# Kernel optimization log

Hardware: AMD Instinct MI355X
Metric: run time of the kernel (lower is better)

## Reference

```python
import jax, jax.numpy as jnp
import numpy as np

EPS_NORM = 1e-5   # o_norm eps
EPS_L2 = 1e-6     # qk l2norm eps
CHUNK = 128       # chunk length for the scan


def _short_conv(x, w):
    # x: [B,T,C], w: [C,K]; causal depthwise conv followed by silu (ShortConvolution)
    K = w.shape[1]
    T = x.shape[1]
    xp = jnp.pad(x, ((0, 0), (K - 1, 0), (0, 0)))
    y = sum(xp[:, i:i + T, :] * w[:, i] for i in range(K))
    return jax.nn.silu(y)


def _l2norm(x):
    return x * jax.lax.rsqrt(jnp.sum(x * x, axis=-1, keepdims=True) + EPS_L2)


def _kda_scan(q, k, v, gk, beta):
    # gated delta rule: S_t = (I - b_t k_t k_t^T) diag(exp(gk_t)) S_{t-1} + b_t k_t v_t^T;  o_t = q_t^T S_t
    # q,k,gk: [B,T,H,Dk]; v: [B,T,H,Dv]; beta: [B,T,H]
    B, T, H, Dk = q.shape
    Dv = v.shape[-1]
    NC = T // CHUNK

    def c4(x):  # [B,T,H,D] -> [NC, CHUNK, B, H, D]
        return jnp.transpose(x.reshape(B, NC, CHUNK, H, x.shape[-1]), (1, 2, 0, 3, 4))

    qc, kc, vc, gc = c4(q), c4(k), c4(v), c4(gk)
    bc = jnp.transpose(beta.reshape(B, NC, CHUNK, H), (1, 2, 0, 3))

    def step(S, inp):  # S: [B,H,Dk,Dv]
        q_t, k_t, v_t, g_t, b_t = inp
        S = S * jnp.exp(g_t)[..., None]                       # per-key-channel decay
        err = v_t - jnp.einsum('bhk,bhkv->bhv', k_t, S)       # delta-rule error
        S = S + b_t[..., None, None] * (k_t[..., None] * err[..., None, :])
        o_t = jnp.einsum('bhk,bhkv->bhv', q_t, S)
        return S, o_t

    @jax.checkpoint
    def chunk_fn(S, xs):
        return jax.lax.scan(step, S, xs)

    S0 = jnp.zeros((B, H, Dk, Dv), q.dtype)
    _, o = jax.lax.scan(chunk_fn, S0, (qc, kc, vc, gc, bc))   # o: [NC, CHUNK, B, H, Dv]
    return jnp.transpose(o.reshape(T, B, H, Dv), (1, 0, 2, 3))


def _forward(hidden_states, q_w, k_w, v_w, q_conv_w, k_conv_w, v_conv_w,
             f_w1, f_w2, b_w, A_log, dt_bias, g_w1, g_w2, g_b2, o_norm_w, o_w):
    B, T, D = hidden_states.shape
    H = A_log.shape[0]
    Dv = o_norm_w.shape[0]
    Dk = q_w.shape[1] // H

    q = _short_conv(hidden_states @ q_w, q_conv_w).reshape(B, T, H, Dk)
    k = _short_conv(hidden_states @ k_w, k_conv_w).reshape(B, T, H, Dk)
    v = _short_conv(hidden_states @ v_w, v_conv_w).reshape(B, T, H, Dv)

    # fused_kda_gate: per-channel log-decay
    g = ((hidden_states @ f_w1) @ f_w2).reshape(B, T, H, Dk)
    gk = -jnp.exp(A_log)[:, None] * jax.nn.softplus(g + dt_bias.reshape(H, Dk))

    beta = jax.nn.sigmoid(hidden_states @ b_w)  # [B,T,H]

    q = _l2norm(q) * (Dk ** -0.5)
    k = _l2norm(k)

    o = _kda_scan(q, k, v, gk, beta)  # [B,T,H,Dv]

    # FusedRMSNormGated(activation='sigmoid')
    gate = ((hidden_states @ g_w1) @ g_w2 + g_b2).reshape(B, T, H, Dv)
    o = o * jax.lax.rsqrt(jnp.mean(o * o, axis=-1, keepdims=True) + EPS_NORM) * o_norm_w
    o = o * jax.nn.sigmoid(gate)

    return o.reshape(B, T, H * Dv) @ o_w


def setup_inputs() -> dict:
    key = jax.random.key(0)
    B, T, D = 2, 4096, 2048
    H, Dk, Dv = 16, 128, 128
    KD, VD = H * Dk, H * Dv
    Kc = 4
    ks = jax.random.split(key, 16)
    s = 0.02
    n = lambda kk, sh: jax.random.normal(kk, sh, jnp.float32) * s
    return dict(
        hidden_states=jax.random.normal(ks[0], (B, T, D), jnp.float32),
        q_w=n(ks[1], (D, KD)), k_w=n(ks[2], (D, KD)), v_w=n(ks[3], (D, VD)),
        q_conv_w=n(ks[4], (KD, Kc)), k_conv_w=n(ks[5], (KD, Kc)), v_conv_w=n(ks[6], (VD, Kc)),
        f_w1=n(ks[7], (D, Dv)), f_w2=n(ks[8], (Dv, KD)),
        b_w=n(ks[9], (D, H)),
        A_log=jnp.log(jax.random.uniform(ks[10], (H,), jnp.float32, 1.0, 16.0)),
        dt_bias=jnp.zeros((KD,), jnp.float32),
        g_w1=n(ks[11], (D, Dv)), g_w2=n(ks[12], (Dv, VD)), g_b2=jnp.zeros((VD,), jnp.float32),
        o_norm_w=jnp.ones((Dv,), jnp.float32),
        o_w=n(ks[13], (VD, D)),
    )


def reference(hidden_states, q_w, k_w, v_w, q_conv_w, k_conv_w, v_conv_w,
              f_w1, f_w2, b_w, A_log, dt_bias, g_w1, g_w2, g_b2, o_norm_w, o_w):
    return _forward(hidden_states, q_w, k_w, v_w, q_conv_w, k_conv_w, v_conv_w,
                    f_w1, f_w2, b_w, A_log, dt_bias, g_w1, g_w2, g_b2, o_norm_w, o_w)
```

## Files before the change

kernel.cpp:

```cpp
#include <hip/hip_runtime.h>
#include <math.h>


constexpr int NB = 2, NT = 4096, ND = 2048, NH = 16, DK = 128, DV = 128;
constexpr int MROWS = NB * NT;
constexpr int BHN   = NB * NH;
constexpr int CCH   = 16;
constexpr int NCH   = NT / CCH;

#define DEV static __device__ __forceinline__

typedef __attribute__((ext_vector_type(8))) short short8;
typedef __attribute__((ext_vector_type(4))) short short4v;
typedef __attribute__((ext_vector_type(4))) float f32x4;

DEV float sigmoidf_(float x) { return 1.0f / (1.0f + expf(-x)); }

DEV float bf2f(unsigned u) { return __uint_as_float(u << 16); }
DEV unsigned f2bf(float f) {
    unsigned u = __float_as_uint(f);
    return (u + 0x7fffu + ((u >> 16) & 1u)) >> 16;
}
DEV unsigned pack2(float a, float b) { return f2bf(a) | (f2bf(b) << 16); }

DEV void gl2lds16(const unsigned short* g, unsigned short* l) {
    __builtin_amdgcn_global_load_lds(
        (const __attribute__((address_space(1))) unsigned int*)g,
        (__attribute__((address_space(3))) unsigned int*)l, 16, 0, 0);
}

template <int CTRL>
DEV float dppadd(float x) {
    int y = __builtin_amdgcn_mov_dpp(__float_as_int(x), CTRL, 0xF, 0xF, true);
    return x + __int_as_float(y);
}
DEV float reduce16f(float x) {
    x = dppadd<0xB1>(x);
    x = dppadd<0x4E>(x);
    x = dppadd<0x141>(x);
    x = dppadd<0x140>(x);
    return x;
}

DEV float4 bflo(uint4 U) {
    return make_float4(bf2f(U.x & 0xffff), bf2f(U.x >> 16),
                       bf2f(U.y & 0xffff), bf2f(U.y >> 16));
}
DEV float4 bfhi(uint4 U) {
    return make_float4(bf2f(U.z & 0xffff), bf2f(U.z >> 16),
                       bf2f(U.w & 0xffff), bf2f(U.w >> 16));
}

DEV f32x4 mfma16(short4v a, short4v b, f32x4 c) {
#if __has_builtin(__builtin_amdgcn_mfma_f32_16x16x16bf16_1k)
    return __builtin_amdgcn_mfma_f32_16x16x16bf16_1k(a, b, c, 0, 0, 0);
#elif __has_builtin(__builtin_amdgcn_mfma_f32_16x16x16_bf16)
    return __builtin_amdgcn_mfma_f32_16x16x16_bf16(a, b, c, 0, 0, 0);
#else
    asm volatile("s_nop 1\n\t"
                 "v_mfma_f32_16x16x16_bf16 %0, %1, %2, %0\n\t"
                 "s_nop 7\n\t"
                 "s_nop 7"
                 : "+v"(c) : "v"(a), "v"(b));
    return c;
#endif
}

template <int OUTBF>
__global__ __launch_bounds__(256) void gemm_bf16(
    const unsigned short* __restrict__ A, const unsigned short* __restrict__ Bt,
    void* __restrict__ Cv, int Md, int Nd, int Kd)
{
    __shared__ unsigned short As[128 * 64];
    __shared__ unsigned short Bs[128 * 64];

    const int nbx = Nd >> 7;
    const int bx = blockIdx.x % nbx;
    const int by = blockIdx.x / nbx;
    const int m0 = by << 7, n0 = bx << 7;
    const int tid = threadIdx.x;
    const int lane = tid & 63, wid = tid >> 6;
    const int wr = wid >> 1, wc = wid & 1;

    const int srow  = tid >> 3;
    const int sslot = (tid & 7) ^ (srow & 7);
    const unsigned short* ag = A  + (size_t)(m0 + srow) * Kd + sslot * 8;
    const unsigned short* bg = Bt + (size_t)(n0 + srow) * Kd + sslot * 8;
    const size_t rstep32 = (size_t)32 * Kd;
    unsigned short* aw = As + wid * 512;
    unsigned short* bw = Bs + wid * 512;

    const int rrow  = lane & 15;
    const int khalf = lane >> 4;
    const int rswz  = rrow & 7;

    f32x4 zf = {0.f, 0.f, 0.f, 0.f};
    f32x4 acc[4][4];
#pragma unroll
    for (int m = 0; m < 4; m++)
#pragma unroll
        for (int n = 0; n < 4; n++) acc[m][n] = zf;

    for (int k0 = 0; k0 < Kd; k0 += 64) {
#pragma unroll
        for (int i = 0; i < 4; i++) {
            gl2lds16(ag + (size_t)i * rstep32 + k0, aw + i * 2048);
            gl2lds16(bg + (size_t)i * rstep32 + k0, bw + i * 2048);
        }
        __syncthreads();
#pragma unroll
        for (int kk = 0; kk < 2; kk++) {
            const int slot = (kk * 4 + khalf) ^ rswz;
            short8 a[4], b[4];
#pragma unroll
            for (int m = 0; m < 4; m++)
                a[m] = *(const short8*)&As[(wr * 64 + m * 16 + rrow) * 64 + slot * 8];
#pragma unroll
            for (int n = 0; n < 4; n++)
                b[n] = *(const short8*)&Bs[(wc * 64 + n * 16 + rrow) * 64 + slot * 8];
#pragma unroll
            for (int m = 0; m < 4; m++)
#pragma unroll
                for (int n = 0; n < 4; n++)
                    acc[m][n] = __builtin_amdgcn_mfma_f32_16x16x32_bf16(
                        a[m], b[n], acc[m][n], 0, 0, 0);
        }
        __syncthreads();
    }

#pragma unroll
    for (int m = 0; m < 4; m++) {
        const int rowb = m0 + wr * 64 + m * 16 + khalf * 4;
#pragma unroll
        for (int n = 0; n < 4; n++) {
            const int col = n0 + wc * 64 + n * 16 + rrow;
#pragma unroll
            for (int r = 0; r < 4; r++) {
                const float v = acc[m][n][r];
                if (OUTBF)
                    ((unsigned short*)Cv)[(size_t)(rowb + r) * Nd + col] =
                        (unsigned short)f2bf(v);
                else
                    ((float*)Cv)[(size_t)(rowb + r) * Nd + col] = v;
            }
        }
    }
}

__global__ __launch_bounds__(256) void wtrans(
    const float* __restrict__ W, unsigned short* __restrict__ Wt, int Kd, int Nd)
{
    __shared__ float T[64][65];
    const int nbk = Kd >> 6;
    const int bk = blockIdx.x % nbk, bn = blockIdx.x / nbk;
    const int k0 = bk << 6, n0 = bn << 6;
    const int tid = threadIdx.x;
    {
        const int r = tid >> 2, cg = tid & 3;
#pragma unroll
        for (int i = 0; i < 4; i++) {
            float4 f = *(const float4*)&W[(size_t)(k0 + r) * Nd + n0 + cg * 16 + i * 4];
            T[r][cg * 16 + i * 4 + 0] = f.x;
            T[r][cg * 16 + i * 4 + 1] = f.y;
            T[r][cg * 16 + i * 4 + 2] = f.z;
            T[r][cg * 16 + i * 4 + 3] = f.w;
        }
    }
    __syncthreads();
    {
        const int n = tid >> 2, kg = tid & 3;
#pragma unroll
        for (int i = 0; i < 2; i++) {
            unsigned o[4];
#pragma unroll
            for (int j = 0; j < 4; j++) {
                const int kk = kg * 16 + i * 8 + 2 * j;
                o[j] = pack2(T[kk][n], T[kk + 1][n]);
            }
            *(uint4*)&Wt[(size_t)(n0 + n) * Kd + k0 + kg * 16 + i * 8] =
                make_uint4(o[0], o[1], o[2], o[3]);
        }
    }
}

__global__ __launch_bounds__(256) void f2bf_k(
    const float* __restrict__ x, unsigned short* __restrict__ y, int n8)
{
    const int i = blockIdx.x * blockDim.x + threadIdx.x;
    if (i < n8) {
        float4 a = *(const float4*)&x[(size_t)i * 8];
        float4 b = *(const float4*)&x[(size_t)i * 8 + 4];
        uint4 o = make_uint4(pack2(a.x, a.y), pack2(a.z, a.w),
                             pack2(b.x, b.y), pack2(b.z, b.w));
        *(uint4*)&y[(size_t)i * 8] = o;
    }
}

template <int MODE>
__global__ __launch_bounds__(256) void conv_silu(
    const unsigned short* __restrict__ pre, const float* __restrict__ cw,
    unsigned short* __restrict__ outp)
{
    const int m = blockIdx.x;
    const int t = m & (NT - 1);
    const int b = m >> 12;
    const int tid = threadIdx.x;
    const int hd = tid * 8;
    const int h  = hd >> 7;
    const int d0 = hd & 127;

    float xr[4][8];
#pragma unroll
    for (int i = 0; i < 4; i++) {
        const int tt = t - 3 + i;
        if (tt >= 0) {
            uint4 u = *(const uint4*)(pre + (size_t)(m - 3 + i) * ND + hd);
            float4 lo = bflo(u), hi = bfhi(u);
            xr[i][0] = lo.x; xr[i][1] = lo.y; xr[i][2] = lo.z; xr[i][3] = lo.w;
            xr[i][4] = hi.x; xr[i][5] = hi.y; xr[i][6] = hi.z; xr[i][7] = hi.w;
        } else {
#pragma unroll
            for (int j = 0; j < 8; j++) xr[i][j] = 0.f;
        }
    }
    float y[8];
    float ssum = 0.f;
#pragma unroll
    for (int j = 0; j < 8; j++) {
        float4 w = *(const float4*)&cw[(size_t)(hd + j) * 4];
        float v = xr[0][j] * w.x + xr[1][j] * w.y + xr[2][j] * w.z + xr[3][j] * w.w;
        v = v * sigmoidf_(v);
        y[j] = v;
        ssum += v * v;
    }
    float scale = 1.f;
    if (MODE >= 1) {
        ssum = reduce16f(ssum);
        scale = rsqrtf(ssum + 1e-6f);
        if (MODE == 2) scale *= 0.08838834764831845f;
    }
    uint4 pk;
    pk.x = pack2(y[0] * scale, y[1] * scale);
    pk.y = pack2(y[2] * scale, y[3] * scale);
    pk.z = pack2(y[4] * scale, y[5] * scale);
    pk.w = pack2(y[6] * scale, y[7] * scale);
    unsigned short* dst = outp + ((size_t)(b * NH + h) * NT + t) * 128 + d0;
    *(uint4*)dst = pk;
}

__global__ __launch_bounds__(256) void gk_k(
    const unsigned short* __restrict__ g, const float* __restrict__ A_log,
    const float* __restrict__ dtb, _Float16* __restrict__ gko)
{
    const int m = blockIdx.x;
    const int t = m & (NT - 1);
    const int b = m >> 12;
    const int tid = threadIdx.x;
    const int hd = tid * 8, h = hd >> 7, d0 = hd & 127;
    const float ea = expf(A_log[h]);
    uint4 u = *(const uint4*)(g + (size_t)m * ND + hd);
    float4 lo = bflo(u), hi = bfhi(u);
    float4 b0 = *(const float4*)&dtb[hd], b1 = *(const float4*)&dtb[hd + 4];
    float xin[8] = {lo.x + b0.x, lo.y + b0.y, lo.z + b0.z, lo.w + b0.w,
                    hi.x + b1.x, hi.y + b1.y, hi.z + b1.z, hi.w + b1.w};
    union { _Float16 h8[8]; uint4 u4; } up;
#pragma unroll
    for (int j = 0; j < 8; j++) {
        float x = xin[j];
        float sp = (x > 20.f) ? x : log1pf(expf(x));
        up.h8[j] = (_Float16)(-ea * sp);
    }
    _Float16* dst = gko + ((size_t)(b * NH + h) * NT + t) * 128 + d0;
    *(uint4*)dst = up.u4;
}

__global__ __launch_bounds__(256) void beta_k(
    const float* __restrict__ hs, const float* __restrict__ bw,
    float* __restrict__ bt)
{
    __shared__ float sh[ND];
    __shared__ float part[16][17];
    const int m = blockIdx.x, tid = threadIdx.x;
    ((float4*)sh)[tid * 2]     = ((const float4*)(hs + (size_t)m * ND))[tid * 2];
    ((float4*)sh)[tid * 2 + 1] = ((const float4*)(hs + (size_t)m * ND))[tid * 2 + 1];
    __syncthreads();
    const int h = tid & 15, seg = tid >> 4;
    float p = 0.f;
#pragma unroll 8
    for (int j = 0; j < 128; j++)
        p += sh[seg * 128 + j] * bw[(size_t)(seg * 128 + j) * 16 + h];
    part[seg][h] = p;
    __syncthreads();
    if (tid < 16) {
        float s = 0.f;
#pragma unroll
        for (int i = 0; i < 16; i++) s += part[i][tid];
        const int t = m & (NT - 1), b = m >> 12;
        bt[(size_t)(b * NH + tid) * NT + t] = sigmoidf_(s);
    }
}

__global__ __launch_bounds__(256) void kda_prep(
    unsigned short* __restrict__ qn, unsigned short* __restrict__ kn,
    unsigned short* __restrict__ vv, unsigned short* __restrict__ gkh,
    const float* __restrict__ bt,
    float* __restrict__ BdB, float* __restrict__ eCB)
{
    __shared__ float cL[16][132];
    __shared__ float kL[16][132];
    __shared__ float qL[16][132];
    __shared__ float kapL[16][132];
    __shared__ float AbL[16][16];
    __shared__ float bL[16];
    __shared__ float sx[16][264];

    const int blk = blockIdx.x;
    const int bh  = blk >> 8;
    const int cc  = blk & 255;
    const int tid = threadIdx.x;
    const size_t ebase  = ((size_t)bh * NT + cc * 16) * 128;
    const size_t chbase = (size_t)bh * NCH + cc;

    if (tid < 16) bL[tid] = bt[(size_t)bh * NT + cc * 16 + tid];

    if (tid < 128) {
        const int d = tid;
        float c = 0.f;
#pragma unroll
        for (int i = 0; i < 16; i++) {
            float g = (float)(((const _Float16*)gkh)[ebase + i * 128 + d]);
            c += g;
            cL[i][d] = c;
            float kv = bf2f(kn[ebase + i * 128 + d]);
            float qv = bf2f(qn[ebase + i * 128 + d]);
            kL[i][d] = kv; qL[i][d] = qv;
            kapL[i][d] = kv * expf(c);
        }
        eCB[chbase * 128 + d] = expf(c);
    }
    __syncthreads();

    if (tid < 128) {
        const int d = tid;
        const float clast = cL[15][d];
        unsigned u[8];
#pragma unroll
        for (int e = 0; e < 8; e++) {
            float v0 = bL[2 * e]     * kL[2 * e][d]     * expf(clast - cL[2 * e][d]);
            float v1 = bL[2 * e + 1] * kL[2 * e + 1][d] * expf(clast - cL[2 * e + 1][d]);
            u[e] = pack2(v0, v1);
        }
        uint4* dst = (uint4*)(gkh + chbase * 2048 + (size_t)d * 16);
        dst[0] = make_uint4(u[0], u[1], u[2], u[3]);
        dst[1] = make_uint4(u[4], u[5], u[6], u[7]);
    }

    const int si = tid >> 4, sj = tid & 15;
    float aAcc = 0.f, bAcc = 0.f;
    if (si >= sj) {
        for (int d4 = 0; d4 < 128; d4 += 4) {
            float4 ci = *(const float4*)&cL[si][d4];
            float4 cj = *(const float4*)&cL[sj][d4];
            float4 ki = *(const float4*)&kL[si][d4];
            float4 kj = *(const float4*)&kL[sj][d4];
            float4 qi = *(const float4*)&qL[si][d4];
            float w;
            w = expf(ci.x - cj.x); aAcc += ki.x * kj.x * w; bAcc += qi.x * kj.x * w;
            w = expf(ci.y - cj.y); aAcc += ki.y * kj.y * w; bAcc += qi.y * kj.y * w;
            w = expf(ci.z - cj.z); aAcc += ki.z * kj.z * w; bAcc += qi.z * kj.z * w;
            w = expf(ci.w - cj.w); aAcc += ki.w * kj.w * w; bAcc += qi.w * kj.w * w;
        }
    }
    if (si > sj) AbL[si][sj] = aAcc * bL[sj];
    BdB[chbase * 256 + si * 16 + sj] = bAcc * bL[sj];
    __syncthreads();

    {
        const int col = tid;
        float x[16];
#pragma unroll
        for (int i = 0; i < 16; i++)
            x[i] = (col < 128) ? kapL[i][col]
                               : bf2f(vv[ebase + (size_t)i * 128 + (col - 128)]);
#pragma unroll
        for (int i = 1; i < 16; i++) {
            float s = x[i];
#pragma unroll
            for (int l = 0; l < 15; l++)
                if (l < i) s -= AbL[i][l] * x[l];
            x[i] = s;
        }
#pragma unroll
        for (int i = 0; i < 16; i++) sx[i][col] = x[i];
    }
    __syncthreads();

    {
        const int row = tid >> 4, d0 = (tid & 15) * 8;
        unsigned pu[4], vu[4], qu[4];
#pragma unroll
        for (int e = 0; e < 4; e++) {
            pu[e] = pack2(-sx[row][d0 + 2 * e], -sx[row][d0 + 2 * e + 1]);
            vu[e] = pack2(sx[row][128 + d0 + 2 * e], sx[row][128 + d0 + 2 * e + 1]);
            qu[e] = pack2(qL[row][d0 + 2 * e]     * expf(cL[row][d0 + 2 * e]),
                          qL[row][d0 + 2 * e + 1] * expf(cL[row][d0 + 2 * e + 1]));
        }
        const size_t ro = ebase + (size_t)row * 128 + d0;
        *(uint4*)(kn + ro) = make_uint4(pu[0], pu[1], pu[2], pu[3]);
        *(uint4*)(vv + ro) = make_uint4(vu[0], vu[1], vu[2], vu[3]);
        *(uint4*)(qn + ro) = make_uint4(qu[0], qu[1], qu[2], qu[3]);
    }
}

__global__ __launch_bounds__(64) void kda_scan2(
    const unsigned short* __restrict__ qn, const unsigned short* __restrict__ kn,
    const unsigned short* __restrict__ vv, const unsigned short* __restrict__ khat,
    const float* __restrict__ BdB, const float* __restrict__ eCB,
    float* __restrict__ osc)
{
    const int bh = blockIdx.x & 31;
    const int vg = blockIdx.x >> 5;
    const int lane = threadIdx.x;
    const int r16 = lane & 15, h4 = lane >> 4;
    const int bb = bh >> 4, hh = bh & 15;

    f32x4 Sm[8];
    short4v Shi[8], Slo[8];
    const short4v z4 = {0, 0, 0, 0};
#pragma unroll
    for (int t = 0; t < 8; t++) {
        Sm[t] = (f32x4){0.f, 0.f, 0.f, 0.f};
        Shi[t] = z4; Slo[t] = z4;
    }

    for (int cc = 0; cc < NCH; cc++) {
        const size_t ebase = ((size_t)bh * NT + cc * 16) * 128;
        const size_t chb = (size_t)bh * NCH + cc;
        short4v P[8], Q[8], KH[8];
        float4 eCt[8];
#pragma unroll
        for (int t = 0; t < 8; t++) {
            P[t]  = *(const short4v*)(kn + ebase + (size_t)r16 * 128 + t * 16 + h4 * 4);
            Q[t]  = *(const short4v*)(qn + ebase + (size_t)r16 * 128 + t * 16 + h4 * 4);
            KH[t] = *(const short4v*)(khat + chb * 2048 + (size_t)(t * 16 + r16) * 16 + h4 * 4);
            eCt[t] = *(const float4*)(eCB + chb * 128 + t * 16 + h4 * 4);
        }
        float4 bd4 = *(const float4*)(BdB + chb * 256 + (size_t)r16 * 16 + h4 * 4);
        short4v bdf;
        bdf[0] = (short)f2bf(bd4.x); bdf[1] = (short)f2bf(bd4.y);
        bdf[2] = (short)f2bf(bd4.z); bdf[3] = (short)f2bf(bd4.w);

        f32x4 accE, accO = {0.f, 0.f, 0.f, 0.f};
#pragma unroll
        for (int r = 0; r < 4; r++)
            accE[r] = bf2f(vv[ebase + (size_t)(h4 * 4 + r) * 128 + vg * 16 + r16]);

#pragma unroll
        for (int t = 0; t < 8; t++) {
            accE = mfma16(P[t], Shi[t], accE);
            accE = mfma16(P[t], Slo[t], accE);
            accO = mfma16(Q[t], Shi[t], accO);
            accO = mfma16(Q[t], Slo[t], accO);
        }
        short4v ef;
        ef[0] = (short)f2bf(accE[0]); ef[1] = (short)f2bf(accE[1]);
        ef[2] = (short)f2bf(accE[2]); ef[3] = (short)f2bf(accE[3]);
        accO = mfma16(bdf, ef, accO);

#pragma unroll
        for (int t = 0; t < 8; t++) {
            f32x4 ns;
            ns[0] = eCt[t].x * Sm[t][0];
            ns[1] = eCt[t].y * Sm[t][1];
            ns[2] = eCt[t].z * Sm[t][2];
            ns[3] = eCt[t].w * Sm[t][3];
            ns = mfma16(KH[t], ef, ns);
            Sm[t] = ns;
            short4v nh, nl;
#pragma unroll
            for (int r = 0; r < 4; r++) {
                unsigned hb = f2bf(ns[r]);
                nh[r] = (short)hb;
                nl[r] = (short)f2bf(ns[r] - bf2f(hb));
            }
            Shi[t] = nh; Slo[t] = nl;
        }

        const size_t obase = ((size_t)bb * NT + cc * 16) * ND + hh * 128 + vg * 16 + r16;
#pragma unroll
        for (int r = 0; r < 4; r++)
            osc[obase + (size_t)(h4 * 4 + r) * ND] = accO[r];
    }
}

__global__ __launch_bounds__(256) void gate_k(
    const float* __restrict__ osc, const unsigned short* __restrict__ gateb,
    const float* __restrict__ gb2, const float* __restrict__ onw,
    unsigned short* __restrict__ ogb)
{
    const int m = blockIdx.x, tid = threadIdx.x;
    const int hd = tid * 8, d0 = hd & 127;
    const float* op = osc + (size_t)m * ND + hd;
    float4 o0 = *(const float4*)op, o1 = *(const float4*)(op + 4);
    float ssum = o0.x * o0.x + o0.y * o0.y + o0.z * o0.z + o0.w * o0.w +
                 o1.x * o1.x + o1.y * o1.y + o1.z * o1.z + o1.w * o1.w;
    ssum = reduce16f(ssum);
    const float r = rsqrtf(ssum * (1.0f / 128.0f) + 1e-5f);
    uint4 gu = *(const uint4*)(gateb + (size_t)m * ND + hd);
    float4 gl = bflo(gu), gh = bfhi(gu);
    float4 b0 = *(const float4*)&gb2[hd], b1 = *(const float4*)&gb2[hd + 4];
    float4 w0 = *(const float4*)&onw[d0], w1 = *(const float4*)&onw[d0 + 4];
    float res[8];
    res[0] = o0.x * r * w0.x * sigmoidf_(gl.x + b0.x);
    res[1] = o0.y * r * w0.y * sigmoidf_(gl.y + b0.y);
    res[2] = o0.z * r * w0.z * sigmoidf_(gl.z + b0.z);
    res[3] = o0.w * r * w0.w * sigmoidf_(gl.w + b0.w);
    res[4] = o1.x * r * w1.x * sigmoidf_(gh.x + b1.x);
    res[5] = o1.y * r * w1.y * sigmoidf_(gh.y + b1.y);
    res[6] = o1.z * r * w1.z * sigmoidf_(gh.z + b1.z);
    res[7] = o1.w * r * w1.w * sigmoidf_(gh.w + b1.w);
    uint4 pk;
    pk.x = pack2(res[0], res[1]); pk.y = pack2(res[2], res[3]);
    pk.z = pack2(res[4], res[5]); pk.w = pack2(res[6], res[7]);
    *(uint4*)(ogb + (size_t)m * ND + hd) = pk;
}

__global__ void diag_fill(float* out, float val, int n) {
    for (int i = blockIdx.x * blockDim.x + threadIdx.x; i < n; i += gridDim.x * blockDim.x)
        out[i] = val;
}

extern "C" void kernel_launch(void* const* d_in, const int* in_sizes, int n_in,
                              void* d_out, int out_size, void* d_ws, size_t ws_size,
                              hipStream_t stream)
{
    const float* hs    = (const float*)d_in[0];
    const float* q_w   = (const float*)d_in[1];
    const float* k_w   = (const float*)d_in[2];
    const float* v_w   = (const float*)d_in[3];
    const float* qcw   = (const float*)d_in[4];
    const float* kcw   = (const float*)d_in[5];
    const float* vcw   = (const float*)d_in[6];
    const float* f_w1  = (const float*)d_in[7];
    const float* f_w2  = (const float*)d_in[8];
    const float* b_w   = (const float*)d_in[9];
    const float* A_log = (const float*)d_in[10];
    const float* dt_b  = (const float*)d_in[11];
    const float* g_w1  = (const float*)d_in[12];
    const float* g_w2  = (const float*)d_in[13];
    const float* g_b2  = (const float*)d_in[14];
    const float* onw   = (const float*)d_in[15];
    const float* o_w   = (const float*)d_in[16];
    float* out = (float*)d_out;

    const size_t SEQ = (size_t)BHN * NT;
    const size_t BF  = SEQ * 128 * 2;
    char* wsb = (char*)d_ws;
    size_t off = 0;
    unsigned short* qn   = (unsigned short*)(wsb + off); off += BF;
    unsigned short* kn   = (unsigned short*)(wsb + off); off += BF;
    unsigned short* vv   = (unsigned short*)(wsb + off); off += BF;
    unsigned short* dc   = (unsigned short*)(wsb + off); off += BF;
    unsigned short* P1   = (unsigned short*)(wsb + off); off += (size_t)MROWS * ND * 2;
    unsigned short* WT   = (unsigned short*)(wsb + off); off += (size_t)ND * ND * 2;
    unsigned short* fw1t = (unsigned short*)(wsb + off); off += (size_t)DK * ND * 2;
    unsigned short* fw2t = (unsigned short*)(wsb + off); off += (size_t)ND * DK * 2;
    unsigned short* gw1t = (unsigned short*)(wsb + off); off += (size_t)DK * ND * 2;
    unsigned short* gw2t = (unsigned short*)(wsb + off); off += (size_t)ND * DK * 2;
    unsigned short* f1b  = (unsigned short*)(wsb + off); off += (size_t)MROWS * DK * 2;
    unsigned short* g1b  = (unsigned short*)(wsb + off); off += (size_t)MROWS * DK * 2;
    float* bt  = (float*)(wsb + off); off += SEQ * 4;
    float* BdB = (float*)(wsb + off); off += (size_t)BHN * NCH * 256 * 4;
    float* eCB = (float*)(wsb + off); off += (size_t)BHN * NCH * 128 * 4;
    unsigned short* ogb = vv;
    unsigned short* hsb = (unsigned short*)d_out;

    if (ws_size < off) {
        diag_fill<<<512, 256, 0, stream>>>(out, 1.0e6f + (float)(ws_size >> 20), out_size);
        return;
    }

    dim3 blk(256);
    auto g2 = [](int Md, int Nd) { return dim3((unsigned)((Md >> 7) * (Nd >> 7))); };
    auto gt = [](int Kd, int Nd) { return dim3((unsigned)((Kd >> 6) * (Nd >> 6))); };

    f2bf_k<<<(MROWS * ND / 8 + 255) / 256, blk, 0, stream>>>(hs, hsb, MROWS * ND / 8);

    wtrans<<<gt(ND, ND), blk, 0, stream>>>(q_w, WT, ND, ND);
    gemm_bf16<1><<<g2(MROWS, ND), blk, 0, stream>>>(hsb, WT, P1, MROWS, ND, ND);
    conv_silu<2><<<MROWS, blk, 0, stream>>>(P1, qcw, qn);
    wtrans<<<gt(ND, ND), blk, 0, stream>>>(k_w, WT, ND, ND);
    gemm_bf16<1><<<g2(MROWS, ND), blk, 0, stream>>>(hsb, WT, P1, MROWS, ND, ND);
    conv_silu<1><<<MROWS, blk, 0, stream>>>(P1, kcw, kn);
    wtrans<<<gt(ND, ND), blk, 0, stream>>>(v_w, WT, ND, ND);
    gemm_bf16<1><<<g2(MROWS, ND), blk, 0, stream>>>(hsb, WT, P1, MROWS, ND, ND);
    conv_silu<0><<<MROWS, blk, 0, stream>>>(P1, vcw, vv);

    wtrans<<<gt(ND, DK), blk, 0, stream>>>(f_w1, fw1t, ND, DK);
    gemm_bf16<1><<<g2(MROWS, DK), blk, 0, stream>>>(hsb, fw1t, f1b, MROWS, DK, ND);
    wtrans<<<gt(DK, ND), blk, 0, stream>>>(f_w2, fw2t, DK, ND);
    gemm_bf16<1><<<g2(MROWS, ND), blk, 0, stream>>>(f1b, fw2t, P1, MROWS, ND, DK);
    gk_k<<<MROWS, blk, 0, stream>>>(P1, A_log, dt_b, (_Float16*)dc);

    wtrans<<<gt(ND, DK), blk, 0, stream>>>(g_w1, gw1t, ND, DK);
    gemm_bf16<1><<<g2(MROWS, DK), blk, 0, stream>>>(hsb, gw1t, g1b, MROWS, DK, ND);
    wtrans<<<gt(DK, ND), blk, 0, stream>>>(g_w2, gw2t, DK, ND);
    gemm_bf16<1><<<g2(MROWS, ND), blk, 0, stream>>>(g1b, gw2t, P1, MROWS, ND, DK);

    beta_k<<<MROWS, blk, 0, stream>>>(hs, b_w, bt);

    kda_prep<<<BHN * NCH, blk, 0, stream>>>(qn, kn, vv, dc, bt, BdB, eCB);
    kda_scan2<<<256, 64, 0, stream>>>(qn, kn, vv, dc, BdB, eCB, out);

    gate_k<<<MROWS, blk, 0, stream>>>(out, P1, g_b2, onw, ogb);

    wtrans<<<gt(ND, ND), blk, 0, stream>>>(o_w, WT, ND, ND);
    gemm_bf16<0><<<g2(MROWS, ND), blk, 0, stream>>>(ogb, WT, out, MROWS, ND, ND);
}
```

Measured before the change: 1.442 ms.

## Double-buffer chunk loads in scan kernel and split MFMA accumulators

Restructures the sequential chunk loop of the recurrent scan kernel so the global loads for the next chunk are issued into a second register set before computing the current chunk. This hides load latency behind the serial MFMA chain. It also splits the E and O accumulations into two independent accumulator chains each, summed at the end, to shorten MFMA dependency chains. The cost is roughly doubled register use for staged operands, which may cause spills or lower occupancy.

```diff
diff --git a/kernel.cpp b/kernel.cpp
--- a/kernel.cpp
+++ b/kernel.cpp
@@ -433,11 +433,10 @@
         Shi[t] = z4; Slo[t] = z4;
     }
 
-    for (int cc = 0; cc < NCH; cc++) {
+    auto loadc = [&](int cc, short4v* P, short4v* Q, short4v* KH,
+                     float4* eCt, short4v& bdf, f32x4& accInit) {
         const size_t ebase = ((size_t)bh * NT + cc * 16) * 128;
         const size_t chb = (size_t)bh * NCH + cc;
-        short4v P[8], Q[8], KH[8];
-        float4 eCt[8];
 #pragma unroll
         for (int t = 0; t < 8; t++) {
             P[t]  = *(const short4v*)(kn + ebase + (size_t)r16 * 128 + t * 16 + h4 * 4);
@@ -446,22 +445,36 @@
             eCt[t] = *(const float4*)(eCB + chb * 128 + t * 16 + h4 * 4);
         }
         float4 bd4 = *(const float4*)(BdB + chb * 256 + (size_t)r16 * 16 + h4 * 4);
-        short4v bdf;
         bdf[0] = (short)f2bf(bd4.x); bdf[1] = (short)f2bf(bd4.y);
         bdf[2] = (short)f2bf(bd4.z); bdf[3] = (short)f2bf(bd4.w);
-
-        f32x4 accE, accO = {0.f, 0.f, 0.f, 0.f};
 #pragma unroll
         for (int r = 0; r < 4; r++)
-            accE[r] = bf2f(vv[ebase + (size_t)(h4 * 4 + r) * 128 + vg * 16 + r16]);
-
-#pragma unroll
-        for (int t = 0; t < 8; t++) {
-            accE = mfma16(P[t], Shi[t], accE);
-            accE = mfma16(P[t], Slo[t], accE);
-            accO = mfma16(Q[t], Shi[t], accO);
-            accO = mfma16(Q[t], Slo[t], accO);
-        }
+            accInit[r] = bf2f(vv[ebase + (size_t)(h4 * 4 + r) * 128 + vg * 16 + r16]);
+    };
+
+    auto compute = [&](int cc, const short4v* P, const short4v* Q,
+                       const short4v* KH, const float4* eCt,
+                       short4v bdf, f32x4 accInit) {
+        f32x4 e0 = accInit, e1 = {0.f, 0.f, 0.f, 0.f};
+        f32x4 o0 = {0.f, 0.f, 0.f, 0.f}, o1 = {0.f, 0.f, 0.f, 0.f};
+#pragma unroll
+        for (int t = 0; t < 8; t += 2) {
+            e0 = mfma16(P[t],     Shi[t],     e0);
+            e1 = mfma16(P[t + 1], Shi[t + 1], e1);
+            o0 = mfma16(Q[t],     Shi[t],     o0);
+            o1 = mfma16(Q[t + 1], Shi[t + 1], o1);
+            e0 = mfma16(P[t],     Slo[t],     e0);
+            e1 = mfma16(P[t + 1], Slo[t + 1], e1);
+            o0 = mfma16(Q[t],     Slo[t],     o0);
+            o1 = mfma16(Q[t + 1], Slo[t + 1], o1);
+        }
+        f32x4 accE;
+        accE[0] = e0[0] + e1[0]; accE[1] = e0[1] + e1[1];
+        accE[2] = e0[2] + e1[2]; accE[3] = e0[3] + e1[3];
+        f32x4 accO;
+        accO[0] = o0[0] + o1[0]; accO[1] = o0[1] + o1[1];
+        accO[2] = o0[2] + o1[2]; accO[3] = o0[3] + o1[3];
+
         short4v ef;
         ef[0] = (short)f2bf(accE[0]); ef[1] = (short)f2bf(accE[1]);
         ef[2] = (short)f2bf(accE[2]); ef[3] = (short)f2bf(accE[3]);
@@ -490,6 +503,20 @@
 #pragma unroll
         for (int r = 0; r < 4; r++)
             osc[obase + (size_t)(h4 * 4 + r) * ND] = accO[r];
+    };
+
+    short4v Pa[8], Qa[8], KHa[8], Pb[8], Qb[8], KHb[8];
+    float4 eCa[8], eCb[8];
+    short4v bda, bdb;
+    f32x4 ia, ib;
+
+    loadc(0, Pa, Qa, KHa, eCa, bda, ia);
+    for (int cc = 0; cc < NCH; cc += 2) {
+        loadc(cc + 1, Pb, Qb, KHb, eCb, bdb, ib);
+        compute(cc, Pa, Qa, KHa, eCa, bda, ia);
+        if (cc + 2 < NCH)
+            loadc(cc + 2, Pa, Qa, KHa, eCa, bda, ia);
+        compute(cc + 1, Pb, Qb, KHb, eCb, bdb, ib);
     }
 }
 
```

Result: faster. 1.306 ms (-9.5%).

## Repack scan operands for 128-bit loads, drop hi/lo split, merge value groups

Applied to the files above, without the earlier changes.

The prep kernel now writes k, q, khat and v in interleaved layouts so the scan loads 8-element short8 vectors instead of 4-element ones. The scan kernel drops the bf16 hi+lo split of the state and uses only the high part, which halves the MFMAs in the recurrence but lowers precision. It also splits the accumulation into two independent chains to shorten dependency latency. The eight value-group blocks per head are merged into one 512-thread block, which launches 32 blocks instead of 256 and cuts the shared per-chunk loads across waves. The risk is accuracy loss from the bf16-only state over 256 chunks.

```diff
diff --git a/kernel.cpp b/kernel.cpp
--- a/kernel.cpp
+++ b/kernel.cpp
@@ -50,6 +50,9 @@
     return make_float4(bf2f(U.z & 0xffff), bf2f(U.z >> 16),
                        bf2f(U.w & 0xffff), bf2f(U.w >> 16));
 }
+
+DEV short4v lo4(short8 v) { short4v r; r[0]=v[0]; r[1]=v[1]; r[2]=v[2]; r[3]=v[3]; return r; }
+DEV short4v hi4(short8 v) { short4v r; r[0]=v[4]; r[1]=v[5]; r[2]=v[6]; r[3]=v[7]; return r; }
 
 DEV f32x4 mfma16(short4v a, short4v b, f32x4 c) {
 #if __has_builtin(__builtin_amdgcn_mfma_f32_16x16x16bf16_1k)
@@ -342,6 +345,7 @@
 
     if (tid < 128) {
         const int d = tid;
+        const int t = d >> 4, rr = d & 15;
         const float clast = cL[15][d];
         unsigned u[8];
 #pragma unroll
@@ -350,9 +354,12 @@
             float v1 = bL[2 * e + 1] * kL[2 * e + 1][d] * expf(clast - cL[2 * e + 1][d]);
             u[e] = pack2(v0, v1);
         }
-        uint4* dst = (uint4*)(gkh + chbase * 2048 + (size_t)d * 16);
-        dst[0] = make_uint4(u[0], u[1], u[2], u[3]);
-        dst[1] = make_uint4(u[4], u[5], u[6], u[7]);
+        unsigned short* base = gkh + chbase * 2048 +
+                               (size_t)(((t >> 1) * 16 + rr) * 32 + (t & 1) * 4);
+        *(uint2*)(base +  0) = make_uint2(u[0], u[1]);
+        *(uint2*)(base +  8) = make_uint2(u[2], u[3]);
+        *(uint2*)(base + 16) = make_uint2(u[4], u[5]);
+        *(uint2*)(base + 24) = make_uint2(u[6], u[7]);
     }
 
     const int si = tid >> 4, sj = tid & 15;
@@ -396,72 +403,92 @@
     __syncthreads();
 
     {
-        const int row = tid >> 4, d0 = (tid & 15) * 8;
-        unsigned pu[4], vu[4], qu[4];
+        const int row = tid >> 4, q16 = tid & 15;
+        const int d0 = q16 * 8;
+        const int t  = q16 >> 1;
+        const int pos0 = (t >> 1) * 32 + (t & 1) * 4 + (q16 & 1) * 16;
+        unsigned pu[4], qu[4];
 #pragma unroll
         for (int e = 0; e < 4; e++) {
             pu[e] = pack2(-sx[row][d0 + 2 * e], -sx[row][d0 + 2 * e + 1]);
-            vu[e] = pack2(sx[row][128 + d0 + 2 * e], sx[row][128 + d0 + 2 * e + 1]);
             qu[e] = pack2(qL[row][d0 + 2 * e]     * expf(cL[row][d0 + 2 * e]),
                           qL[row][d0 + 2 * e + 1] * expf(cL[row][d0 + 2 * e + 1]));
         }
-        const size_t ro = ebase + (size_t)row * 128 + d0;
-        *(uint4*)(kn + ro) = make_uint4(pu[0], pu[1], pu[2], pu[3]);
-        *(uint4*)(vv + ro) = make_uint4(vu[0], vu[1], vu[2], vu[3]);
-        *(uint4*)(qn + ro) = make_uint4(qu[0], qu[1], qu[2], qu[3]);
-    }
-}
-
-__global__ __launch_bounds__(64) void kda_scan2(
+        unsigned short* kb = kn + ebase + (size_t)row * 128 + pos0;
+        unsigned short* qb = qn + ebase + (size_t)row * 128 + pos0;
+        *(uint2*)(kb)     = make_uint2(pu[0], pu[1]);
+        *(uint2*)(kb + 8) = make_uint2(pu[2], pu[3]);
+        *(uint2*)(qb)     = make_uint2(qu[0], qu[1]);
+        *(uint2*)(qb + 8) = make_uint2(qu[2], qu[3]);
+    }
+    if (tid < 128) {
+        const int c = tid;
+        unsigned u2[8];
+#pragma unroll
+        for (int e = 0; e < 8; e++)
+            u2[e] = pack2(sx[2 * e][128 + c], sx[2 * e + 1][128 + c]);
+        unsigned short* vb = vv + ebase + (size_t)c * 16;
+        *(uint4*)(vb)     = make_uint4(u2[0], u2[1], u2[2], u2[3]);
+        *(uint4*)(vb + 8) = make_uint4(u2[4], u2[5], u2[6], u2[7]);
+    }
+}
+
+__global__ __launch_bounds__(512) void kda_scan3(
     const unsigned short* __restrict__ qn, const unsigned short* __restrict__ kn,
     const unsigned short* __restrict__ vv, const unsigned short* __restrict__ khat,
     const float* __restrict__ BdB, const float* __restrict__ eCB,
     float* __restrict__ osc)
 {
-    const int bh = blockIdx.x & 31;
-    const int vg = blockIdx.x >> 5;
-    const int lane = threadIdx.x;
+    const int bh = blockIdx.x;
+    const int vg = threadIdx.x >> 6;
+    const int lane = threadIdx.x & 63;
     const int r16 = lane & 15, h4 = lane >> 4;
     const int bb = bh >> 4, hh = bh & 15;
 
     f32x4 Sm[8];
-    short4v Shi[8], Slo[8];
+    short4v Shi[8];
     const short4v z4 = {0, 0, 0, 0};
 #pragma unroll
-    for (int t = 0; t < 8; t++) {
-        Sm[t] = (f32x4){0.f, 0.f, 0.f, 0.f};
-        Shi[t] = z4; Slo[t] = z4;
-    }
+    for (int t = 0; t < 8; t++) { Sm[t] = (f32x4){0.f, 0.f, 0.f, 0.f}; Shi[t] = z4; }
 
     for (int cc = 0; cc < NCH; cc++) {
         const size_t ebase = ((size_t)bh * NT + cc * 16) * 128;
         const size_t chb = (size_t)bh * NCH + cc;
-        short4v P[8], Q[8], KH[8];
+
+        short8 Pp[4], Qp[4], KHp[4];
+#pragma unroll
+        for (int m = 0; m < 4; m++) {
+            Pp[m]  = *(const short8*)(kn + ebase + (size_t)r16 * 128 + m * 32 + h4 * 8);
+            Qp[m]  = *(const short8*)(qn + ebase + (size_t)r16 * 128 + m * 32 + h4 * 8);
+            KHp[m] = *(const short8*)(khat + chb * 2048 + (size_t)(m * 16 + r16) * 32 + h4 * 8);
+        }
+        short4v vvt = *(const short4v*)(vv + ebase + (size_t)(vg * 16 + r16) * 16 + h4 * 4);
         float4 eCt[8];
 #pragma unroll
-        for (int t = 0; t < 8; t++) {
-            P[t]  = *(const short4v*)(kn + ebase + (size_t)r16 * 128 + t * 16 + h4 * 4);
-            Q[t]  = *(const short4v*)(qn + ebase + (size_t)r16 * 128 + t * 16 + h4 * 4);
-            KH[t] = *(const short4v*)(khat + chb * 2048 + (size_t)(t * 16 + r16) * 16 + h4 * 4);
+        for (int t = 0; t < 8; t++)
             eCt[t] = *(const float4*)(eCB + chb * 128 + t * 16 + h4 * 4);
-        }
         float4 bd4 = *(const float4*)(BdB + chb * 256 + (size_t)r16 * 16 + h4 * 4);
         short4v bdf;
         bdf[0] = (short)f2bf(bd4.x); bdf[1] = (short)f2bf(bd4.y);
         bdf[2] = (short)f2bf(bd4.z); bdf[3] = (short)f2bf(bd4.w);
 
-        f32x4 accE, accO = {0.f, 0.f, 0.f, 0.f};
-#pragma unroll
-        for (int r = 0; r < 4; r++)
-            accE[r] = bf2f(vv[ebase + (size_t)(h4 * 4 + r) * 128 + vg * 16 + r16]);
-
-#pragma unroll
-        for (int t = 0; t < 8; t++) {
-            accE = mfma16(P[t], Shi[t], accE);
-            accE = mfma16(P[t], Slo[t], accE);
-            accO = mfma16(Q[t], Shi[t], accO);
-            accO = mfma16(Q[t], Slo[t], accO);
-        }
+        f32x4 e0, e1 = {0.f, 0.f, 0.f, 0.f};
+        f32x4 o0 = {0.f, 0.f, 0.f, 0.f}, o1 = {0.f, 0.f, 0.f, 0.f};
+        e0[0] = bf2f((unsigned short)vvt[0]); e0[1] = bf2f((unsigned short)vvt[1]);
+        e0[2] = bf2f((unsigned short)vvt[2]); e0[3] = bf2f((unsigned short)vvt[3]);
+#pragma unroll
+        for (int m = 0; m < 4; m++) {
+            e0 = mfma16(lo4(Pp[m]), Shi[2 * m],     e0);
+            e1 = mfma16(hi4(Pp[m]), Shi[2 * m + 1], e1);
+            o0 = mfma16(lo4(Qp[m]), Shi[2 * m],     o0);
+            o1 = mfma16(hi4(Qp[m]), Shi[2 * m + 1], o1);
+        }
+        f32x4 accE, accO;
+        accE[0] = e0[0] + e1[0]; accE[1] = e0[1] + e1[1];
+        accE[2] = e0[2] + e1[2]; accE[3] = e0[3] + e1[3];
+        accO[0] = o0[0] + o1[0]; accO[1] = o0[1] + o1[1];
+        accO[2] = o0[2] + o1[2]; accO[3] = o0[3] + o1[3];
+
         short4v ef;
         ef[0] = (short)f2bf(accE[0]); ef[1] = (short)f2bf(accE[1]);
         ef[2] = (short)f2bf(accE[2]); ef[3] = (short)f2bf(accE[3]);
@@ -469,21 +496,18 @@
 
 #pragma unroll
         for (int t = 0; t < 8; t++) {
+            const short4v khf = (t & 1) ? hi4(KHp[t >> 1]) : lo4(KHp[t >> 1]);
             f32x4 ns;
             ns[0] = eCt[t].x * Sm[t][0];
             ns[1] = eCt[t].y * Sm[t][1];
             ns[2] = eCt[t].z * Sm[t][2];
             ns[3] = eCt[t].w * Sm[t][3];
-            ns = mfma16(KH[t], ef, ns);
+            ns = mfma16(khf, ef, ns);
             Sm[t] = ns;
-            short4v nh, nl;
-#pragma unroll
-            for (int r = 0; r < 4; r++) {
-                unsigned hb = f2bf(ns[r]);
-                nh[r] = (short)hb;
-                nl[r] = (short)f2bf(ns[r] - bf2f(hb));
-            }
-            Shi[t] = nh; Slo[t] = nl;
+            short4v nh;
+            nh[0] = (short)f2bf(ns[0]); nh[1] = (short)f2bf(ns[1]);
+            nh[2] = (short)f2bf(ns[2]); nh[3] = (short)f2bf(ns[3]);
+            Shi[t] = nh;
         }
 
         const size_t obase = ((size_t)bb * NT + cc * 16) * ND + hh * 128 + vg * 16 + r16;
@@ -610,7 +634,7 @@
     beta_k<<<MROWS, blk, 0, stream>>>(hs, b_w, bt);
 
     kda_prep<<<BHN * NCH, blk, 0, stream>>>(qn, kn, vv, dc, bt, BdB, eCB);
-    kda_scan2<<<256, 64, 0, stream>>>(qn, kn, vv, dc, BdB, eCB, out);
+    kda_scan3<<<BHN, 512, 0, stream>>>(qn, kn, vv, dc, BdB, eCB, out);
 
     gate_k<<<MROWS, blk, 0, stream>>>(out, P1, g_b2, onw, ogb);
 
```

Result: slower. 1.792 ms (+24.2%).
